# Performance work log

Measured on AMD Instinct MI355X. Metric: run time of the kernel, lower is better.

The kernel has to match this reference:

```python
import jax, jax.numpy as jnp
import numpy as np

N_MODULES = 32
POINTER_DIM = 64
CONTENT_DIM = 256
N_CYCLES = 1
EPS = 1e-42  # denormal but representable in float32, as in original


def setup_inputs() -> dict:
    key = jax.random.key(0)
    ks = jax.random.split(key, 8)
    B, T, M, P, C = 16, 128, N_MODULES, POINTER_DIM, CONTENT_DIM
    pointers = jax.random.normal(ks[0], (B, T, P), dtype=jnp.float32)
    contents = jax.random.normal(ks[1], (B, T, C), dtype=jnp.float32)
    # learned parameters (kaiming-uniform-like scaling)
    receivers = jax.random.uniform(ks[2], (M, P), minval=-1.0, maxval=1.0) / np.sqrt(P)
    memories = jax.random.uniform(ks[3], (M, C, C), minval=-1.0, maxval=1.0) / np.sqrt(C)
    # per-module routing MLP: Linear(C+P -> P), ReLU, Linear(P -> P), ReLU
    W1 = jax.random.uniform(ks[4], (M, C + P, P), minval=-1.0, maxval=1.0) / np.sqrt(C + P)
    b1 = jnp.zeros((M, P), dtype=jnp.float32)
    W2 = jax.random.uniform(ks[5], (M, P, P), minval=-1.0, maxval=1.0) / np.sqrt(P)
    b2 = jnp.zeros((M, P), dtype=jnp.float32)
    return {"pointers": pointers, "contents": contents, "receivers": receivers,
            "memories": memories, "W1": W1, "b1": b1, "W2": W2, "b2": b2}


def _cycle(pointers, contents, mems, receivers, W1, b1, W2, b2):
    # in-weightings: relu(tanh(receivers @ pointers^T)) -> [B, M, T]
    w_in = jax.nn.relu(jnp.tanh(jnp.einsum('mp,btp->bmt', receivers, pointers)))
    # weighted gather-reduce over tokens
    eff_c = jnp.einsum('bmt,btc->bmc', w_in, contents)   # [B, M, C]
    eff_p = jnp.einsum('bmt,btp->bmp', w_in, pointers)   # [B, M, P]
    # memory read: batched matvec
    out_c = jnp.einsum('bmcd,bmd->bmc', mems, eff_c)     # [B, M, C]
    # per-module routing MLP (batched over modules with einsum)
    routing_in = jnp.concatenate([eff_p, eff_c], axis=-1)            # [B, M, P+C]
    h = jax.nn.relu(jnp.einsum('bmi,mio->bmo', routing_in, W1) + b1)  # [B, M, P]
    out_p = jax.nn.relu(jnp.einsum('bmi,mio->bmo', h, W2) + b2)       # [B, M, P]
    # out-weightings over modules
    w_out = jax.nn.relu(jnp.tanh(jnp.einsum('bmp,bnp->bmn', out_p, out_p)))  # [B, M, M]
    eff_out_c = jnp.einsum('bmn,bnc->bmc', w_out, out_c)  # [B, M, C]
    # outer-product memory update
    normed_in = eff_c / (jnp.sum(eff_c * eff_c, axis=-1, keepdims=True) + EPS)
    perfect = jnp.einsum('bmc,bmd->bmcd', eff_out_c, normed_in)  # [B, M, C, C]
    mems = 0.5 * (mems + perfect)
    return out_p, out_c, mems


def reference(pointers, contents, receivers, memories, W1, b1, W2, b2):
    B = pointers.shape[0]
    mems = jnp.broadcast_to(memories[None], (B,) + memories.shape)
    for _ in range(N_CYCLES):
        pointers, contents, mems = _cycle(pointers, contents, mems,
                                          receivers, W1, b1, W2, b2)
    return pointers, contents, mems
```

## Files before the change

kernel.cpp:

```cpp
#include <hip/hip_runtime.h>
#include <math.h>

#define BB 16
#define TT 128
#define MM 32
#define PP 64
#define CC 256

typedef float f32x4 __attribute__((ext_vector_type(4)));

__global__ __launch_bounds__(512) void K1_front(
        const float* __restrict__ pointers,
        const float* __restrict__ contents,
        const float* __restrict__ receivers,
        const float* __restrict__ memories,
        const float* __restrict__ W1,
        const float* __restrict__ b1,
        const float* __restrict__ W2,
        const float* __restrict__ b2,
        float* __restrict__ nrm_ws,
        float* __restrict__ outp_g,
        float* __restrict__ outc_g) {
    const int bm = blockIdx.x;
    const int b = bm >> 5, m = bm & 31;
    const int tid = threadIdx.x;
    const int lane = tid & 63, w = tid >> 6;

    __shared__ float w_in[TT];
    __shared__ __align__(16) float ri[PP + CC];
    __shared__ float partc[4][CC];
    __shared__ float part8[8][PP];
    __shared__ float h[PP];
    __shared__ float outc_s[CC];
    __shared__ float red[4];

    {
        const int t = tid >> 2, q = tid & 3;
        const float4* pr4 = reinterpret_cast<const float4*>(pointers + (b * TT + t) * PP + q * 16);
        const float4* rc4 = reinterpret_cast<const float4*>(receivers + m * PP + q * 16);
        float s = 0.f;
        #pragma unroll
        for (int k = 0; k < 4; ++k) {
            float4 v = pr4[k], rv = rc4[k];
            s += v.x * rv.x + v.y * rv.y + v.z * rv.z + v.w * rv.w;
        }
        s += __shfl_xor(s, 1, 64);
        s += __shfl_xor(s, 2, 64);
        if (q == 0) {
            float th = tanhf(s);
            w_in[t] = th > 0.f ? th : 0.f;
        }
    }
    __syncthreads();
    {
        const int cp = tid & 127, g = tid >> 7;
        const float2* cb2 = reinterpret_cast<const float2*>(contents + (b * TT + g * 32) * CC) + cp;
        float2 acc = {0.f, 0.f};
        #pragma unroll 8
        for (int t = 0; t < 32; ++t) {
            float2 v = cb2[t * 128];
            const float ww = w_in[g * 32 + t];
            acc.x += ww * v.x;
            acc.y += ww * v.y;
        }
        partc[g][2 * cp]     = acc.x;
        partc[g][2 * cp + 1] = acc.y;
    }
    {
        const int p = tid & 63, g = tid >> 6;
        const float* pb = pointers + (b * TT + g * 16) * PP + p;
        float acc = 0.f;
        #pragma unroll
        for (int t = 0; t < 16; ++t) acc += w_in[g * 16 + t] * pb[t * PP];
        part8[g][p] = acc;
    }
    __syncthreads();
    float ecv = 0.f;
    if (tid < CC) {
        ecv = partc[0][tid] + partc[1][tid] + partc[2][tid] + partc[3][tid];
        ri[PP + tid] = ecv;
        float v = ecv * ecv;
        #pragma unroll
        for (int off = 32; off; off >>= 1) v += __shfl_xor(v, off, 64);
        if (lane == 0) red[w] = v;
    } else if (tid < CC + PP) {
        const int p = tid - CC;
        float a = 0.f;
        #pragma unroll
        for (int g = 0; g < 8; ++g) a += part8[g][p];
        ri[p] = a;
    }
    __syncthreads();
    if (tid < CC) {
        const float ss = red[0] + red[1] + red[2] + red[3];
        nrm_ws[bm * CC + tid] = ecv / (ss + 1e-42f);
    }

    {
        const int g = lane >> 4, j = lane & 15;
        float4 e_reg[4];
        #pragma unroll
        for (int k = 0; k < 4; ++k)
            e_reg[k] = *reinterpret_cast<const float4*>(&ri[PP + 4 * (j + 16 * k)]);
        const float4* mem4 = reinterpret_cast<const float4*>(memories) + m * (CC * CC / 4);
        #pragma unroll
        for (int i = 0; i < 8; ++i) {
            const int c = w * 32 + i * 4 + g;
            const float4* row4 = mem4 + c * 64;
            float s = 0.f;
            #pragma unroll
            for (int k = 0; k < 4; ++k) {
                float4 mv = row4[j + 16 * k];
                s += mv.x * e_reg[k].x + mv.y * e_reg[k].y
                   + mv.z * e_reg[k].z + mv.w * e_reg[k].w;
            }
            s += __shfl_xor(s, 1, 64);
            s += __shfl_xor(s, 2, 64);
            s += __shfl_xor(s, 4, 64);
            s += __shfl_xor(s, 8, 64);
            if (j == 0) outc_s[c] = s;
        }
    }

    {
        const float* w1 = W1 + m * 320 * 64;
        float acc = 0.f;
        const int i0 = w * 40;
        #pragma unroll 8
        for (int i = i0; i < i0 + 40; ++i) acc += ri[i] * w1[i * 64 + lane];
        __syncthreads();
        part8[w][lane] = acc;
    }
    __syncthreads();
    if (tid < PP) {
        float s = b1[m * PP + tid];
        #pragma unroll
        for (int g = 0; g < 8; ++g) s += part8[g][tid];
        h[tid] = s > 0.f ? s : 0.f;
    }
    __syncthreads();
    {
        const float* w2 = W2 + m * 64 * 64;
        float acc = 0.f;
        const int i0 = w * 8;
        #pragma unroll
        for (int i = i0; i < i0 + 8; ++i) acc += h[i] * w2[i * 64 + lane];
        part8[w][lane] = acc;
    }
    __syncthreads();
    if (tid < PP) {
        float s = b2[m * PP + tid];
        #pragma unroll
        for (int g = 0; g < 8; ++g) s += part8[g][tid];
        outp_g[bm * PP + tid] = s > 0.f ? s : 0.f;
    }
    if (tid < CC) outc_g[bm * CC + tid] = outc_s[tid];
}

__global__ __launch_bounds__(256) void K3_fused(
        const float* __restrict__ memories,
        const float* __restrict__ outp_g,
        const float* __restrict__ outc_g,
        const float* __restrict__ nrm_ws,
        float* __restrict__ mems_out) {
    const int gid = blockIdx.x;
    const int b = gid >> 7;
    const int m = (gid >> 2) & 31, cs = gid & 3;
    const int bm = b * MM + m;
    const int tid = threadIdx.x;
    const int lane = tid & 63, w = tid >> 6;

    __shared__ float wout_s[MM];
    __shared__ float eoc_s[64];

    {
        const int n = tid >> 3, j = tid & 7;
        const float* opm = outp_g + bm * PP + j * 8;
        const float* opn = outp_g + (b * MM + n) * PP + j * 8;
        float s = 0.f;
        #pragma unroll
        for (int k = 0; k < 8; ++k) s += opm[k] * opn[k];
        s += __shfl_xor(s, 1, 64);
        s += __shfl_xor(s, 2, 64);
        s += __shfl_xor(s, 4, 64);
        if (j == 0) {
            float th = tanhf(s);
            wout_s[n] = th > 0.f ? th : 0.f;
        }
    }
    const float4 nv = *reinterpret_cast<const float4*>(nrm_ws + bm * CC + lane * 4);
    __syncthreads();
    {
        const int c_local = tid >> 2, k = tid & 3;
        const int c = cs * 64 + c_local;
        const float* cb = outc_g + (b * MM + k * 8) * CC + c;
        float s = 0.f;
        #pragma unroll
        for (int kk = 0; kk < 8; ++kk)
            s += wout_s[k * 8 + kk] * cb[kk * CC];
        s += __shfl_xor(s, 1, 64);
        s += __shfl_xor(s, 2, 64);
        if (k == 0) eoc_s[c_local] = s;
    }
    __syncthreads();

    const f32x4* mem4 = reinterpret_cast<const f32x4*>(memories) + (m * CC + cs * 64) * 64;
    f32x4* out4 = reinterpret_cast<f32x4*>(mems_out) + (bm * CC + cs * 64) * 64;

    #pragma unroll
    for (int it = 0; it < 16; ++it) {
        const int idx = it * 256 + tid;
        const float e = eoc_s[it * 4 + w];
        f32x4 mv = mem4[idx];
        f32x4 o;
        o.x = 0.5f * (mv.x + e * nv.x);
        o.y = 0.5f * (mv.y + e * nv.y);
        o.z = 0.5f * (mv.z + e * nv.z);
        o.w = 0.5f * (mv.w + e * nv.w);
        out4[idx] = o;
    }
}

extern "C" void kernel_launch(void* const* d_in, const int* in_sizes, int n_in,
                              void* d_out, int out_size, void* d_ws, size_t ws_size,
                              hipStream_t stream) {
    const float* pointers  = (const float*)d_in[0];
    const float* contents  = (const float*)d_in[1];
    const float* receivers = (const float*)d_in[2];
    const float* memories  = (const float*)d_in[3];
    const float* W1 = (const float*)d_in[4];
    const float* b1 = (const float*)d_in[5];
    const float* W2 = (const float*)d_in[6];
    const float* b2 = (const float*)d_in[7];

    float* out      = (float*)d_out;
    float* outp_g   = out;
    float* outc_g   = out + 32768;
    float* mems_out = out + 32768 + 131072;

    float* nrm = (float*)d_ws;

    hipLaunchKernelGGL(K1_front, dim3(BB * MM), dim3(512), 0, stream,
                       pointers, contents, receivers, memories, W1, b1, W2, b2,
                       nrm, outp_g, outc_g);
    hipLaunchKernelGGL(K3_fused, dim3(BB * MM * 4), dim3(256), 0, stream,
                       memories, outp_g, outc_g, nrm, mems_out);
}
```

Before: 47.01 us.

## Split out-weighting and eff_out_c computation into a per-batch routing kernel

Moves the w_out (out_p·out_p^T, tanh, relu) and eff_out_c mixing out of the 2048-block streaming kernel into a new 16-block kernel. That kernel stages out_p and out_c in shared memory and writes eff_out_c to workspace. Previously each streaming block recomputed its own w_out row and re-read out_p and out_c, which was redundant work. The cost is an extra kernel launch and a low-parallelism 16-block stage on the critical path.

```diff
diff --git a/kernel.cpp b/kernel.cpp
--- a/kernel.cpp
+++ b/kernel.cpp
@@ -157,10 +157,55 @@
     if (tid < CC) outc_g[bm * CC + tid] = outc_s[tid];
 }
 
-__global__ __launch_bounds__(256) void K3_fused(
-        const float* __restrict__ memories,
+__global__ __launch_bounds__(1024) void K2_route(
         const float* __restrict__ outp_g,
         const float* __restrict__ outc_g,
+        float* __restrict__ eoc_ws) {
+    const int b = blockIdx.x;
+    const int tid = threadIdx.x;
+    __shared__ float op[MM][PP + 1];
+    __shared__ float oc[MM][CC];
+    __shared__ float wout[MM][MM];
+
+    #pragma unroll
+    for (int k = 0; k < 2; ++k) {
+        const int i = k * 1024 + tid;
+        op[i >> 6][i & 63] = outp_g[b * MM * PP + i];
+    }
+    {
+        const float4* src = reinterpret_cast<const float4*>(outc_g + b * MM * CC);
+        #pragma unroll
+        for (int k = 0; k < 2; ++k) {
+            const int i = k * 1024 + tid;
+            *reinterpret_cast<float4*>(&oc[i >> 6][(i & 63) * 4]) = src[i];
+        }
+    }
+    __syncthreads();
+    {
+        const int m = tid >> 5, n = tid & 31;
+        float s = 0.f;
+        #pragma unroll 16
+        for (int p = 0; p < PP; ++p) s += op[m][p] * op[n][p];
+        float th = tanhf(s);
+        wout[m][n] = th > 0.f ? th : 0.f;
+    }
+    __syncthreads();
+    {
+        const int g = tid >> 8, c = tid & 255;
+        #pragma unroll
+        for (int mm = 0; mm < 8; ++mm) {
+            const int m = g * 8 + mm;
+            float s = 0.f;
+            #pragma unroll 8
+            for (int n = 0; n < MM; ++n) s += wout[m][n] * oc[n][c];
+            eoc_ws[(b * MM + m) * CC + c] = s;
+        }
+    }
+}
+
+__global__ __launch_bounds__(256) void K3_stream(
+        const float* __restrict__ memories,
+        const float* __restrict__ eoc_ws,
         const float* __restrict__ nrm_ws,
         float* __restrict__ mems_out) {
     const int gid = blockIdx.x;
@@ -170,38 +215,9 @@
     const int tid = threadIdx.x;
     const int lane = tid & 63, w = tid >> 6;
 
-    __shared__ float wout_s[MM];
     __shared__ float eoc_s[64];
-
-    {
-        const int n = tid >> 3, j = tid & 7;
-        const float* opm = outp_g + bm * PP + j * 8;
-        const float* opn = outp_g + (b * MM + n) * PP + j * 8;
-        float s = 0.f;
-        #pragma unroll
-        for (int k = 0; k < 8; ++k) s += opm[k] * opn[k];
-        s += __shfl_xor(s, 1, 64);
-        s += __shfl_xor(s, 2, 64);
-        s += __shfl_xor(s, 4, 64);
-        if (j == 0) {
-            float th = tanhf(s);
-            wout_s[n] = th > 0.f ? th : 0.f;
-        }
-    }
     const float4 nv = *reinterpret_cast<const float4*>(nrm_ws + bm * CC + lane * 4);
-    __syncthreads();
-    {
-        const int c_local = tid >> 2, k = tid & 3;
-        const int c = cs * 64 + c_local;
-        const float* cb = outc_g + (b * MM + k * 8) * CC + c;
-        float s = 0.f;
-        #pragma unroll
-        for (int kk = 0; kk < 8; ++kk)
-            s += wout_s[k * 8 + kk] * cb[kk * CC];
-        s += __shfl_xor(s, 1, 64);
-        s += __shfl_xor(s, 2, 64);
-        if (k == 0) eoc_s[c_local] = s;
-    }
+    if (tid < 64) eoc_s[tid] = eoc_ws[bm * CC + cs * 64 + tid];
     __syncthreads();
 
     const f32x4* mem4 = reinterpret_cast<const f32x4*>(memories) + (m * CC + cs * 64) * 64;
@@ -238,11 +254,15 @@
     float* outc_g   = out + 32768;
     float* mems_out = out + 32768 + 131072;
 
-    float* nrm = (float*)d_ws;
+    float* ws  = (float*)d_ws;
+    float* nrm = ws;
+    float* eoc = ws + 131072;
 
     hipLaunchKernelGGL(K1_front, dim3(BB * MM), dim3(512), 0, stream,
                        pointers, contents, receivers, memories, W1, b1, W2, b2,
                        nrm, outp_g, outc_g);
-    hipLaunchKernelGGL(K3_fused, dim3(BB * MM * 4), dim3(256), 0, stream,
-                       memories, outp_g, outc_g, nrm, mems_out);
-}
+    hipLaunchKernelGGL(K2_route, dim3(BB), dim3(1024), 0, stream,
+                       outp_g, outc_g, eoc);
+    hipLaunchKernelGGL(K3_stream, dim3(BB * MM * 4), dim3(256), 0, stream,
+                       memories, eoc, nrm, mems_out);
+}
```

Result: slower. 55.55 us (+18.2%).

## Reuse memory tile in registers across four batches in K3

Applied to the files above, without the earlier changes.

K3 now launches 512 blocks instead of 2048. Each block loads its 64-row slice of the module memory into registers once and reuses it for four batch indices (b0, b0+4, b0+8, b0+12), writing four output tiles. This cuts repeated reads of the shared memories tensor, leaving the kernel dominated by output writes. In exchange it uses more registers per thread (16 float4), has fewer blocks to hide latency with, and adds per-batch barriers inside the loop.

```diff
diff --git a/kernel.cpp b/kernel.cpp
--- a/kernel.cpp
+++ b/kernel.cpp
@@ -163,61 +163,68 @@
         const float* __restrict__ outc_g,
         const float* __restrict__ nrm_ws,
         float* __restrict__ mems_out) {
-    const int gid = blockIdx.x;
-    const int b = gid >> 7;
-    const int m = (gid >> 2) & 31, cs = gid & 3;
-    const int bm = b * MM + m;
+    const int gid0 = blockIdx.x;
+    const int b0 = gid0 >> 7;
+    const int m = (gid0 >> 2) & 31, cs = gid0 & 3;
     const int tid = threadIdx.x;
     const int lane = tid & 63, w = tid >> 6;
 
     __shared__ float wout_s[MM];
     __shared__ float eoc_s[64];
 
-    {
-        const int n = tid >> 3, j = tid & 7;
-        const float* opm = outp_g + bm * PP + j * 8;
-        const float* opn = outp_g + (b * MM + n) * PP + j * 8;
-        float s = 0.f;
-        #pragma unroll
-        for (int k = 0; k < 8; ++k) s += opm[k] * opn[k];
-        s += __shfl_xor(s, 1, 64);
-        s += __shfl_xor(s, 2, 64);
-        s += __shfl_xor(s, 4, 64);
-        if (j == 0) {
-            float th = tanhf(s);
-            wout_s[n] = th > 0.f ? th : 0.f;
-        }
-    }
-    const float4 nv = *reinterpret_cast<const float4*>(nrm_ws + bm * CC + lane * 4);
-    __syncthreads();
-    {
-        const int c_local = tid >> 2, k = tid & 3;
-        const int c = cs * 64 + c_local;
-        const float* cb = outc_g + (b * MM + k * 8) * CC + c;
-        float s = 0.f;
-        #pragma unroll
-        for (int kk = 0; kk < 8; ++kk)
-            s += wout_s[k * 8 + kk] * cb[kk * CC];
-        s += __shfl_xor(s, 1, 64);
-        s += __shfl_xor(s, 2, 64);
-        if (k == 0) eoc_s[c_local] = s;
-    }
-    __syncthreads();
-
     const f32x4* mem4 = reinterpret_cast<const f32x4*>(memories) + (m * CC + cs * 64) * 64;
-    f32x4* out4 = reinterpret_cast<f32x4*>(mems_out) + (bm * CC + cs * 64) * 64;
-
+    f32x4 mv[16];
     #pragma unroll
-    for (int it = 0; it < 16; ++it) {
-        const int idx = it * 256 + tid;
-        const float e = eoc_s[it * 4 + w];
-        f32x4 mv = mem4[idx];
-        f32x4 o;
-        o.x = 0.5f * (mv.x + e * nv.x);
-        o.y = 0.5f * (mv.y + e * nv.y);
-        o.z = 0.5f * (mv.z + e * nv.z);
-        o.w = 0.5f * (mv.w + e * nv.w);
-        out4[idx] = o;
+    for (int k = 0; k < 16; ++k) mv[k] = mem4[k * 256 + tid];
+
+    for (int k4 = 0; k4 < 4; ++k4) {
+        const int b = b0 + 4 * k4;
+        const int bm = b * MM + m;
+        if (k4) __syncthreads();
+
+        const float4 nv = *reinterpret_cast<const float4*>(nrm_ws + bm * CC + lane * 4);
+
+        {
+            const int n = tid >> 3, j = tid & 7;
+            const float* opm = outp_g + bm * PP + j * 8;
+            const float* opn = outp_g + (b * MM + n) * PP + j * 8;
+            float s = 0.f;
+            #pragma unroll
+            for (int k = 0; k < 8; ++k) s += opm[k] * opn[k];
+            s += __shfl_xor(s, 1, 64);
+            s += __shfl_xor(s, 2, 64);
+            s += __shfl_xor(s, 4, 64);
+            if (j == 0) {
+                float th = tanhf(s);
+                wout_s[n] = th > 0.f ? th : 0.f;
+            }
+        }
+        __syncthreads();
+        {
+            const int c_local = tid >> 2, k = tid & 3;
+            const int c = cs * 64 + c_local;
+            const float* cb = outc_g + (b * MM + k * 8) * CC + c;
+            float s = 0.f;
+            #pragma unroll
+            for (int kk = 0; kk < 8; ++kk)
+                s += wout_s[k * 8 + kk] * cb[kk * CC];
+            s += __shfl_xor(s, 1, 64);
+            s += __shfl_xor(s, 2, 64);
+            if (k == 0) eoc_s[c_local] = s;
+        }
+        __syncthreads();
+
+        f32x4* out4 = reinterpret_cast<f32x4*>(mems_out) + (bm * CC + cs * 64) * 64;
+        #pragma unroll
+        for (int k = 0; k < 16; ++k) {
+            const float e = eoc_s[k * 4 + w];
+            f32x4 o;
+            o.x = 0.5f * (mv[k].x + e * nv.x);
+            o.y = 0.5f * (mv[k].y + e * nv.y);
+            o.z = 0.5f * (mv[k].z + e * nv.z);
+            o.w = 0.5f * (mv[k].w + e * nv.w);
+            out4[k * 256 + tid] = o;
+        }
     }
 }
 
@@ -243,6 +250,6 @@
     hipLaunchKernelGGL(K1_front, dim3(BB * MM), dim3(512), 0, stream,
                        pointers, contents, receivers, memories, W1, b1, W2, b2,
                        nrm, outp_g, outc_g);
-    hipLaunchKernelGGL(K3_fused, dim3(BB * MM * 4), dim3(256), 0, stream,
+    hipLaunchKernelGGL(K3_fused, dim3(512), dim3(256), 0, stream,
                        memories, outp_g, outc_g, nrm, mems_out);
 }
```

Result: faster. 43.38 us (median of 2 runs) (-7.7%).
